# Kernel tuning notes

Measured on AMD Instinct MI355X. Metric: run time of the kernel, lower is better.

The kernel has to match this reference:

```python
import jax, jax.numpy as jnp
import numpy as np

EPS = 1e-5

def layer_norm(x, g, b):
    m = x.mean(-1, keepdims=True)
    v = ((x - m) ** 2).mean(-1, keepdims=True)
    return (x - m) / jnp.sqrt(v + EPS) * g + b

def lstm(x_sbd, W_ih, W_hh, b_ih, b_hh):
    # x_sbd: (S, B, D); PyTorch gate order i, f, g, o
    S, B, D = x_sbd.shape
    H = W_hh.shape[1]
    h0 = jnp.zeros((B, H), x_sbd.dtype)
    c0 = jnp.zeros((B, H), x_sbd.dtype)
    def step(carry, x_t):
        h, c = carry
        gates = x_t @ W_ih.T + b_ih + h @ W_hh.T + b_hh
        i, f, g, o = jnp.split(gates, 4, axis=-1)
        c = jax.nn.sigmoid(f) * c + jax.nn.sigmoid(i) * jnp.tanh(g)
        h = jax.nn.sigmoid(o) * jnp.tanh(c)
        return (h, c), h
    (hL, _), hs = jax.lax.scan(step, (h0, c0), x_sbd)
    return hs, hL  # (S,B,H), (B,H)

def setup_inputs():
    key = jax.random.key(0)
    ks = jax.random.split(key, 20)
    B, S, D, V = 64, 1024, 128, 50000
    sc = 1.0 / np.sqrt(D)
    r = lambda k, shp, s=sc: (jax.random.normal(k, shp, jnp.float32) * s)
    return {
        "new_list": jax.random.randint(ks[0], (B, S), 0, V, jnp.int32),
        "new_mask": jnp.ones((B, S), jnp.float32),
        "aspect": jax.random.randint(ks[1], (B, 1), 0, V, jnp.int32),
        "gpunum": 0,
        "emb": r(ks[2], (V, D), 0.02),
        "W_ih": r(ks[3], (4 * D, D)),
        "W_hh": r(ks[4], (4 * D, D)),
        "b_ih": jnp.zeros((4 * D,), jnp.float32),
        "b_hh": jnp.zeros((4 * D,), jnp.float32),
        "an_g": jnp.ones((D,), jnp.float32),
        "an_b": jnp.zeros((D,), jnp.float32),
        "hn_g": jnp.ones((D,), jnp.float32),
        "hn_b": jnp.zeros((D,), jnp.float32),
        "W_att": r(ks[5], (D, D)),
        "W_aw": r(ks[6], (1, D)),
        "W_rout": r(ks[7], (D, D)),
        "W_hout": r(ks[8], (D, D)),
        "W_cls": r(ks[9], (2, D)),
        "b_cls": jnp.zeros((2,), jnp.float32),
    }

def reference(new_list, new_mask, aspect, gpunum, emb, W_ih, W_hh, b_ih, b_hh,
              an_g, an_b, hn_g, hn_b, W_att, W_aw, W_rout, W_hout, W_cls, b_cls):
    # embed, seq-major for LSTM
    x = emb[new_list.T]                      # (S, B, D)
    hidden_output, h_L = lstm(x, W_ih, W_hh, b_ih, b_hh)
    aspect_emb = emb[aspect]                 # (B, 1, D)
    aspect_emb = layer_norm(aspect_emb, an_g, an_b)
    hidden_output = layer_norm(hidden_output, hn_g, hn_b)
    hid = jnp.transpose(hidden_output, (1, 0, 2))  # (B, S, D)
    # circular convolution along hidden dim via FFT (batched; replaces host scipy loop)
    M = jnp.real(jnp.fft.ifft(jnp.fft.fft(hid, axis=-1) * jnp.fft.fft(aspect_emb, axis=-1), axis=-1)).astype(hid.dtype)
    # self-attention: key=M, value=hid, mask applied before softmax (as in original)
    QK = jnp.tanh(M @ W_att.T)               # (B, S, D)
    QK = new_mask[..., None] * QK
    weight = jax.nn.softmax(QK @ W_aw.T, axis=1)  # (B, S, 1)
    r = jnp.einsum('bs,bsd->bd', weight[..., 0], hid)
    r = jnp.tanh(r @ W_rout.T + h_L @ W_hout.T)
    result = jax.nn.softmax(r @ W_cls.T + b_cls, axis=-1)
    return (result, r)
```

## Files before the change

kernel.cpp:

```cpp
#include <hip/hip_runtime.h>

typedef __attribute__((ext_vector_type(8))) short s16x8;
typedef __attribute__((ext_vector_type(4))) float f32x4;
typedef __attribute__((ext_vector_type(4))) unsigned short u16x4;
typedef __attribute__((ext_vector_type(8))) unsigned short u16x8;

#define PAD 136
#define LPAD 144

__device__ __forceinline__ unsigned short f2bf(float f){
  union{float f;unsigned u;} v; v.f=f;
  unsigned r=v.u + 0x7fffu + ((v.u>>16)&1u);
  return (unsigned short)(r>>16);
}
__device__ __forceinline__ float bf2f(unsigned short u){
  union{unsigned u;float f;} v; v.u=((unsigned)u)<<16; return v.f;
}
__device__ __forceinline__ float ubits2f(unsigned u){
  union{unsigned u;float f;} v; v.u=u; return v.f;
}
__device__ __forceinline__ float rcp_(float x){ return __builtin_amdgcn_rcpf(x); }
__device__ __forceinline__ float e2_(float x){ return __builtin_amdgcn_exp2f(x); }
__device__ __forceinline__ float tanh_(float x){ return 1.f-2.f*rcp_(1.f+e2_(x*2.885390082f)); }

__device__ __forceinline__ void mfma128(const unsigned short* As, const unsigned short* Bs, f32x4 acc[4][2]){
  const int tid=threadIdx.x, w=tid>>6, l=tid&63;
  const int wm=w>>2, wn=w&3, lr=l&15, lk=(l>>4)*8;
#pragma unroll
  for(int kc=0;kc<4;++kc){
    const int ko=kc*32+lk;
    s16x8 a[4], bb[2];
#pragma unroll
    for(int mt=0;mt<4;++mt) a[mt]=*(const s16x8*)(As+(wm*64+mt*16+lr)*PAD+ko);
#pragma unroll
    for(int nt=0;nt<2;++nt) bb[nt]=*(const s16x8*)(Bs+(wn*32+nt*16+lr)*PAD+ko);
#pragma unroll
    for(int mt=0;mt<4;++mt)
#pragma unroll
      for(int nt=0;nt<2;++nt)
        acc[mt][nt]=__builtin_amdgcn_mfma_f32_16x16x32_bf16(a[mt],bb[nt],acc[mt][nt],0,0,0);
  }
}

__global__ __launch_bounds__(256) void k_cvt(const float* __restrict__ w, unsigned short* __restrict__ o, int n){
  int i = blockIdx.x*256 + threadIdx.x;
  if (i<n) o[i] = f2bf(w[i]);
}

__global__ __launch_bounds__(512) void k_aspg(const int* __restrict__ aspect, const float* __restrict__ emb,
    const float* __restrict__ ang, const float* __restrict__ anb, const float* __restrict__ watt,
    unsigned short* __restrict__ gt){
  __shared__ unsigned short As[128*PAD];
  __shared__ unsigned short Bs[128*PAD];
  __shared__ float a_ln[128];
  __shared__ float stat[2];
  const int b=blockIdx.x, tid=threadIdx.x;
  if (tid<128) a_ln[tid] = emb[(size_t)aspect[b]*128 + tid];
  __syncthreads();
  if (tid==0){
    float s=0.f,q=0.f;
    for(int d=0;d<128;++d){ float v=a_ln[d]; s+=v; q+=v*v; }
    float m=s*(1.f/128.f);
    stat[0]=m; stat[1]=__builtin_amdgcn_rsqf(q*(1.f/128.f)-m*m+1e-5f);
  }
  __syncthreads();
  if (tid<128) a_ln[tid] = (a_ln[tid]-stat[0])*stat[1]*ang[tid]+anb[tid];
  __syncthreads();
  {
    int k=tid>>2, dq=(tid&3)*32;
    for(int d=dq; d<dq+32; ++d) As[k*PAD+d]=f2bf(a_ln[(d-k)&127]);
  }
  {
    int i=tid>>2, kq=(tid&3)*32;
    const f32x4* src=(const f32x4*)(watt+(size_t)i*128+kq);
#pragma unroll
    for(int j=0;j<8;++j){ f32x4 v=src[j]; u16x4 o;
#pragma unroll
      for(int q=0;q<4;++q) o[q]=f2bf(v[q]);
      *(u16x4*)(Bs+i*PAD+kq+4*j)=o; }
  }
  __syncthreads();
  f32x4 z={0.f,0.f,0.f,0.f};
  f32x4 acc[4][2]={{z,z},{z,z},{z,z},{z,z}};
  mfma128(As,Bs,acc);
  const int w=tid>>6,l=tid&63,wm=w>>2,wn=w&3,lr=l&15,lg=l>>4;
#pragma unroll
  for(int mt=0;mt<4;++mt)
#pragma unroll
    for(int nt=0;nt<2;++nt){
      int k0=wm*64+mt*16+lg*4;
      int n=wn*32+nt*16+lr;
      u16x4 o;
#pragma unroll
      for(int r=0;r<4;++r) o[r]=f2bf(acc[mt][nt][r]);
      *(u16x4*)(gt+(size_t)b*16384+n*128+k0)=o;
    }
}

__global__ __launch_bounds__(512) void k_xw(const int* __restrict__ new_list, const float* __restrict__ emb,
    const float* __restrict__ wih, const float* __restrict__ bih, const float* __restrict__ bhh,
    unsigned short* __restrict__ xw){
  __shared__ unsigned short As[128*PAD];
  __shared__ unsigned short Bs[128*PAD];
  const int tid=threadIdx.x;
  const int m0=blockIdx.x*128, n0=blockIdx.y*128;
  {
    int i=tid>>2, kq=(tid&3)*32;
    int m=m0+i, t=m>>6, b=m&63;
    int tok=new_list[b*1024+t];
    const f32x4* src=(const f32x4*)(emb+(size_t)tok*128+kq);
#pragma unroll
    for(int j=0;j<8;++j){ f32x4 v=src[j]; u16x4 o;
#pragma unroll
      for(int q=0;q<4;++q) o[q]=f2bf(v[q]);
      *(u16x4*)(As+i*PAD+kq+4*j)=o; }
  }
  {
    int i=tid>>2, kq=(tid&3)*32;
    const f32x4* src=(const f32x4*)(wih+(size_t)(n0+i)*128+kq);
#pragma unroll
    for(int j=0;j<8;++j){ f32x4 v=src[j]; u16x4 o;
#pragma unroll
      for(int q=0;q<4;++q) o[q]=f2bf(v[q]);
      *(u16x4*)(Bs+i*PAD+kq+4*j)=o; }
  }
  __syncthreads();
  f32x4 z={0.f,0.f,0.f,0.f};
  f32x4 acc[4][2]={{z,z},{z,z},{z,z},{z,z}};
  mfma128(As,Bs,acc);
  const int w=tid>>6,l=tid&63,wm=w>>2,wn=w&3,lr=l&15,lg=l>>4;
#pragma unroll
  for(int nt=0;nt<2;++nt){
    int n=n0+wn*32+nt*16+lr;
    float bias=bih[n]+bhh[n];
#pragma unroll
    for(int mt=0;mt<4;++mt){
      int m_=m0+wm*64+mt*16+lg*4;
      int t=m_>>6, b0=m_&63;
      u16x4 o;
#pragma unroll
      for(int r=0;r<4;++r) o[r]=f2bf(acc[mt][nt][r]+bias);
      *(u16x4*)(xw+(((size_t)t*16+(b0>>2))*512+n)*4)=o;
    }
  }
}

__global__ __launch_bounds__(512) void k_lstm(const unsigned short* __restrict__ xw,
    const unsigned short* __restrict__ whh,
    unsigned short* __restrict__ hraw, float* __restrict__ hL){
  __shared__ unsigned short hbuf[2][4*LPAD];
  const int tid=threadIdx.x, w=tid>>6, l=tid&63, lr=l&15, lg=l>>4;
  const int blk=blockIdx.x, bb=blk*4;
  const int cb=w*16+lr;
  s16x8 wf[4][4];
#pragma unroll
  for(int g=0;g<4;++g)
#pragma unroll
    for(int kc=0;kc<4;++kc)
      wf[g][kc]=*(const s16x8*)(whh+(size_t)(g*128+cb)*128+kc*32+lg*8);
  for(int i=tid;i<2*4*LPAD;i+=512) ((unsigned short*)hbuf)[i]=0;
  __syncthreads();
  const unsigned short* x0 = xw + (size_t)blk*2048;
  int xofs[4];
#pragma unroll
  for(int g=0;g<4;++g) xofs[g]=((g*128+cb)<<2)+lg;
  unsigned short px[4], p1[4];
#pragma unroll
  for(int g=0;g<4;++g) px[g]=x0[xofs[g]];
#pragma unroll
  for(int g=0;g<4;++g) p1[g]=x0[32768+xofs[g]];
  unsigned short* hrp=hraw+((size_t)(bb+lg)<<17)+cb;
  float cc=0.f, hh=0.f;
  int cur=0;
  const float L2E=1.442695041f;
  for(int t=0;t<1024;++t){
    const unsigned short* hc=hbuf[cur];
    s16x8 af[4];
#pragma unroll
    for(int kc=0;kc<4;++kc) af[kc]=*(const s16x8*)(hc+(lr>>2)*LPAD+kc*32+lg*8);
    { int t2=t+2<1024?t+2:1023;
      const unsigned short* xq=x0+(size_t)t2*32768;
      unsigned short pn[4];
#pragma unroll
      for(int g=0;g<4;++g) pn[g]=xq[xofs[g]];
      f32x4 z={0.f,0.f,0.f,0.f};
      f32x4 acc[4]={z,z,z,z};
#pragma unroll
      for(int kc=0;kc<4;++kc)
#pragma unroll
        for(int g=0;g<4;++g)
          acc[g]=__builtin_amdgcn_mfma_f32_16x16x32_bf16(af[kc],wf[g][kc],acc[g],0,0,0);
      float ga[4];
#pragma unroll
      for(int g=0;g<4;++g){
        ga[g]=acc[g][0]+ubits2f(((unsigned)px[g])<<16);
        px[g]=p1[g]; p1[g]=pn[g];
      }
      float gg=__builtin_amdgcn_fmed3f(ga[2],-30.f,30.f);
      float ei=e2_(ga[0]*-L2E), eg=e2_(gg*(-2.f*L2E));
      float sitg=rcp_((1.f+ei)*(1.f+eg))*(1.f-eg);
      float sf=rcp_(1.f+e2_(ga[1]*-L2E));
      cc=fmaf(sf,cc,sitg);
      float cl=__builtin_amdgcn_fmed3f(cc,-30.f,30.f);
      float E=e2_(cl*(2.f*L2E)), eo=e2_(ga[3]*-L2E);
      hh=(E-1.f)*rcp_((1.f+eo)*(E+1.f));
    }
    unsigned p;
    asm("v_cvt_pk_bf16_f32 %0, %1, %2":"=v"(p):"v"(hh),"v"(hh));
    unsigned short hb=(unsigned short)(p&0xffffu);
    hbuf[cur^1][lg*LPAD+cb]=hb;
    hrp[(size_t)t<<7]=hb;
    asm volatile("s_waitcnt lgkmcnt(0)\n\ts_barrier" ::: "memory");
    cur^=1;
  }
  hL[(size_t)(bb+lg)*128+cb]=hh;
}

__global__ __launch_bounds__(512) void k_scores(const unsigned short* __restrict__ hraw,
    const unsigned short* __restrict__ gt, const float* __restrict__ hng, const float* __restrict__ hnb,
    const float* __restrict__ waw, const float* __restrict__ mask,
    unsigned short* __restrict__ hln, float* __restrict__ scores){
  __shared__ unsigned short As[128*PAD];
  __shared__ unsigned short Bs[128*PAD];
  __shared__ float redS[128][4];
  __shared__ float redQ[128][4];
  __shared__ float red[128][4];
  const int b=blockIdx.x>>3, s0=(blockIdx.x&7)*128;
  const int tid=threadIdx.x;
  const int i=tid>>2, kq=(tid&3)*32;
  u16x8 hv[4];
  {
    const u16x8* src=(const u16x8*)(hraw+((size_t)b*1024+s0+i)*128+kq);
    float s=0.f,q=0.f;
#pragma unroll
    for(int j=0;j<4;++j){ hv[j]=src[j];
#pragma unroll
      for(int e=0;e<8;++e){ float x=bf2f(hv[j][e]); s+=x; q+=x*x; } }
    redS[i][tid&3]=s; redQ[i][tid&3]=q;
  }
  {
    const u16x4* src=(const u16x4*)(gt+(size_t)b*16384+i*128+kq);
#pragma unroll
    for(int j=0;j<8;++j) *(u16x4*)(Bs+i*PAD+kq+4*j)=src[j];
  }
  __syncthreads();
  {
    float s=redS[i][0]+redS[i][1]+redS[i][2]+redS[i][3];
    float q=redQ[i][0]+redQ[i][1]+redQ[i][2]+redQ[i][3];
    float m=s*(1.f/128.f);
    float inv=__builtin_amdgcn_rsqf(q*(1.f/128.f)-m*m+1e-5f);
    unsigned short* dst=hln+((size_t)b*1024+s0+i)*128+kq;
#pragma unroll
    for(int j=0;j<4;++j){ u16x8 o;
#pragma unroll
      for(int e=0;e<8;++e){ int d=kq+j*8+e;
        float x=(bf2f(hv[j][e])-m)*inv*hng[d]+hnb[d];
        o[e]=f2bf(x); }
      *(u16x8*)(As+i*PAD+kq+8*j)=o;
      *(u16x8*)(dst+8*j)=o;
    }
  }
  __syncthreads();
  f32x4 z={0.f,0.f,0.f,0.f};
  f32x4 acc[4][2]={{z,z},{z,z},{z,z},{z,z}};
  mfma128(As,Bs,acc);
  const int w=tid>>6,l=tid&63,wm=w>>2,wn=w&3,lr=l&15,lg=l>>4;
  const float w0=waw[wn*32+lr], w1=waw[wn*32+16+lr];
#pragma unroll
  for(int mt=0;mt<4;++mt){
    f32x4 p4;
#pragma unroll
    for(int r=0;r<4;++r) p4[r]=tanh_(acc[mt][0][r])*w0+tanh_(acc[mt][1][r])*w1;
#pragma unroll
    for(int m=1;m<16;m<<=1){
#pragma unroll
      for(int r=0;r<4;++r) p4[r]+=__shfl_xor(p4[r],m,64);
    }
    if (lr==0){
#pragma unroll
      for(int r=0;r<4;++r) red[wm*64+mt*16+lg*4+r][wn]=p4[r];
    }
  }
  __syncthreads();
  if (tid<128){
    float sc=red[tid][0]+red[tid][1]+red[tid][2]+red[tid][3];
    sc*=mask[b*1024+s0+tid];
    scores[b*1024+s0+tid]=sc;
  }
}

__global__ __launch_bounds__(256) void k_wsum(const float* __restrict__ scores,
    const unsigned short* __restrict__ hln, float* __restrict__ rpre){
  __shared__ float wl[1024];
  __shared__ float red[256];
  __shared__ float part[8][32];
  const int b=blockIdx.x>>2, d0=(blockIdx.x&3)*32;
  const int tid=threadIdx.x;
  float v[4]; float lm=-1e30f;
#pragma unroll
  for(int q=0;q<4;++q){ v[q]=scores[b*1024+tid+256*q]; lm=fmaxf(lm,v[q]); }
  red[tid]=lm; __syncthreads();
  for(int st=128;st;st>>=1){ if(tid<st) red[tid]=fmaxf(red[tid],red[tid+st]); __syncthreads(); }
  const float mx=red[0]; __syncthreads();
  float ls=0.f;
#pragma unroll
  for(int q=0;q<4;++q){ v[q]=e2_((v[q]-mx)*1.442695041f); ls+=v[q]; }
  red[tid]=ls; __syncthreads();
  for(int st=128;st;st>>=1){ if(tid<st) red[tid]+=red[tid+st]; __syncthreads(); }
  const float inv=rcp_(red[0]);
#pragma unroll
  for(int q=0;q<4;++q) wl[tid+256*q]=v[q]*inv;
  __syncthreads();
  const int d=tid&31, sg=tid>>5;
  float acc=0.f;
  const unsigned short* hp=hln+(size_t)b*131072+d0+d;
  for(int s=sg*128;s<sg*128+128;++s) acc+=wl[s]*bf2f(hp[(size_t)s*128]);
  part[sg][d]=acc; __syncthreads();
  if (tid<32){
    float a=0.f;
#pragma unroll
    for(int g=0;g<8;++g) a+=part[g][tid];
    rpre[b*128+d0+tid]=a;
  }
}

__global__ __launch_bounds__(128) void k_final(const float* __restrict__ rpre, const float* __restrict__ hLp,
    const float* __restrict__ wrout, const float* __restrict__ whout, const float* __restrict__ wcls,
    const float* __restrict__ bcls, float* __restrict__ out){
  __shared__ float rv[128], hv[128], cred[4];
  const int b=blockIdx.x, n=threadIdx.x;
  rv[n]=rpre[b*128+n]; hv[n]=hLp[b*128+n];
  __syncthreads();
  float a=0.f;
  const float* wr=wrout+(size_t)n*128;
  const float* wh=whout+(size_t)n*128;
  for(int k=0;k<128;++k) a+=rv[k]*wr[k]+hv[k]*wh[k];
  const float rr=tanh_(a);
  out[128+b*128+n]=rr;
  float p0=rr*wcls[n], p1=rr*wcls[128+n];
#pragma unroll
  for(int m=1;m<64;m<<=1){ p0+=__shfl_xor(p0,m,64); p1+=__shfl_xor(p1,m,64); }
  if ((n&63)==0){ cred[(n>>6)*2]=p0; cred[(n>>6)*2+1]=p1; }
  __syncthreads();
  if (n==0){
    float l0=cred[0]+cred[2]+bcls[0], l1=cred[1]+cred[3]+bcls[1];
    float m=fmaxf(l0,l1);
    float e0=e2_((l0-m)*1.442695041f), e1=e2_((l1-m)*1.442695041f);
    float s=rcp_(e0+e1);
    out[b*2]=e0*s; out[b*2+1]=e1*s;
  }
}

extern "C" void kernel_launch(void* const* d_in, const int* in_sizes, int n_in,
                              void* d_out, int out_size, void* d_ws, size_t ws_size,
                              hipStream_t stream) {
  (void)in_sizes; (void)n_in; (void)out_size; (void)ws_size;
  const int*   new_list=(const int*)d_in[0];
  const float* new_mask=(const float*)d_in[1];
  const int*   aspect  =(const int*)d_in[2];
  const float* emb   =(const float*)d_in[4];
  const float* W_ih  =(const float*)d_in[5];
  const float* W_hh  =(const float*)d_in[6];
  const float* b_ih  =(const float*)d_in[7];
  const float* b_hh  =(const float*)d_in[8];
  const float* an_g  =(const float*)d_in[9];
  const float* an_b  =(const float*)d_in[10];
  const float* hn_g  =(const float*)d_in[11];
  const float* hn_b  =(const float*)d_in[12];
  const float* W_att =(const float*)d_in[13];
  const float* W_aw  =(const float*)d_in[14];
  const float* W_rout=(const float*)d_in[15];
  const float* W_hout=(const float*)d_in[16];
  const float* W_cls =(const float*)d_in[17];
  const float* b_cls =(const float*)d_in[18];
  float* out=(float*)d_out;
  char* ws=(char*)d_ws;
  unsigned short* xw    =(unsigned short*)(ws);
  unsigned short* hraw  =(unsigned short*)(ws+67108864);
  unsigned short* hln   =(unsigned short*)(ws+83886080);
  unsigned short* gt    =(unsigned short*)(ws+100663296);
  unsigned short* whh   =(unsigned short*)(ws+102760448);
  float*          scores=(float*)(ws+102891520);
  float*          hLb   =(float*)(ws+103153664);
  float*          rpre  =(float*)(ws+103186432);
  k_cvt   <<<dim3(256),    dim3(256), 0, stream>>>(W_hh, whh, 512*128);
  k_aspg  <<<dim3(64),     dim3(512), 0, stream>>>(aspect, emb, an_g, an_b, W_att, gt);
  k_xw    <<<dim3(512,4),  dim3(512), 0, stream>>>(new_list, emb, W_ih, b_ih, b_hh, xw);
  k_lstm  <<<dim3(16),     dim3(512), 0, stream>>>(xw, whh, hraw, hLb);
  k_scores<<<dim3(512),    dim3(512), 0, stream>>>(hraw, gt, hn_g, hn_b, W_aw, new_mask, hln, scores);
  k_wsum  <<<dim3(256),    dim3(256), 0, stream>>>(scores, hln, rpre);
  k_final <<<dim3(64),     dim3(128), 0, stream>>>(rpre, hLb, W_rout, W_hout, W_cls, b_cls, out);
}
```

Before: 578.7 us.

## Batch LSTM hidden-state stores through an 8-step LDS ring and prescale gate inputs

The LSTM kernel now keeps the last eight hidden states in an LDS ring buffer. Every eight steps it writes them to global memory as 16-byte vector stores, replacing one 2-byte scattered global store per step. The input projection and W_hh conversion fold the -log2(e) and -2log2(e) factors into the stored bf16 values, which removes a multiply per gate in the serial recurrence. The price is an extra barrier every eight steps, plus extra rounding because the scaled values are kept in bf16.

New measurement: 1.088 ms. +88.0%, slower.

```diff
diff --git a/kernel.cpp b/kernel.cpp
--- a/kernel.cpp
+++ b/kernel.cpp
@@ -7,6 +7,7 @@
 
 #define PAD 136
 #define LPAD 144
+#define SSTR (4*LPAD+2)
 
 __device__ __forceinline__ unsigned short f2bf(float f){
   union{float f;unsigned u;} v; v.f=f;
@@ -44,7 +45,11 @@
 
 __global__ __launch_bounds__(256) void k_cvt(const float* __restrict__ w, unsigned short* __restrict__ o, int n){
   int i = blockIdx.x*256 + threadIdx.x;
-  if (i<n) o[i] = f2bf(w[i]);
+  if (i<n){
+    int g=(i>>14)&3;
+    float s=(g==2)?-2.885390082f:-1.442695041f;
+    o[i] = f2bf(w[i]*s);
+  }
 }
 
 __global__ __launch_bounds__(512) void k_aspg(const int* __restrict__ aspect, const float* __restrict__ emb,
@@ -133,13 +138,14 @@
   for(int nt=0;nt<2;++nt){
     int n=n0+wn*32+nt*16+lr;
     float bias=bih[n]+bhh[n];
+    float s=((n>>7)==2)?-2.885390082f:-1.442695041f;
 #pragma unroll
     for(int mt=0;mt<4;++mt){
       int m_=m0+wm*64+mt*16+lg*4;
       int t=m_>>6, b0=m_&63;
       u16x4 o;
 #pragma unroll
-      for(int r=0;r<4;++r) o[r]=f2bf(acc[mt][nt][r]+bias);
+      for(int r=0;r<4;++r) o[r]=f2bf((acc[mt][nt][r]+bias)*s);
       *(u16x4*)(xw+(((size_t)t*16+(b0>>2))*512+n)*4)=o;
     }
   }
@@ -148,7 +154,7 @@
 __global__ __launch_bounds__(512) void k_lstm(const unsigned short* __restrict__ xw,
     const unsigned short* __restrict__ whh,
     unsigned short* __restrict__ hraw, float* __restrict__ hL){
-  __shared__ unsigned short hbuf[2][4*LPAD];
+  __shared__ unsigned short hbuf[8][SSTR];
   const int tid=threadIdx.x, w=tid>>6, l=tid&63, lr=l&15, lg=l>>4;
   const int blk=blockIdx.x, bb=blk*4;
   const int cb=w*16+lr;
@@ -158,7 +164,7 @@
 #pragma unroll
     for(int kc=0;kc<4;++kc)
       wf[g][kc]=*(const s16x8*)(whh+(size_t)(g*128+cb)*128+kc*32+lg*8);
-  for(int i=tid;i<2*4*LPAD;i+=512) ((unsigned short*)hbuf)[i]=0;
+  for(int i=tid;i<8*SSTR;i+=512) ((unsigned short*)hbuf)[i]=0;
   __syncthreads();
   const unsigned short* x0 = xw + (size_t)blk*2048;
   int xofs[4];
@@ -169,49 +175,54 @@
   for(int g=0;g<4;++g) px[g]=x0[xofs[g]];
 #pragma unroll
   for(int g=0;g<4;++g) p1[g]=x0[32768+xofs[g]];
-  unsigned short* hrp=hraw+((size_t)(bb+lg)<<17)+cb;
+  const int ro=tid>>7, ss=(tid>>4)&7, c0=(tid&15)*8;
+  const unsigned short* hls=&hbuf[ss][ro*LPAD+c0];
+  unsigned short* hst = hraw + ((size_t)(bb+ro)<<17) + (ss<<7) + c0;
   float cc=0.f, hh=0.f;
-  int cur=0;
-  const float L2E=1.442695041f;
   for(int t=0;t<1024;++t){
-    const unsigned short* hc=hbuf[cur];
+    if ((t&7)==0 && t){
+      u16x8 v=*(const u16x8*)hls;
+      *(u16x8*)(hst + ((size_t)(t-8)<<7)) = v;
+      asm volatile("s_waitcnt lgkmcnt(0)\n\ts_barrier" ::: "memory");
+    }
+    const unsigned short* hc=hbuf[(t+7)&7];
     s16x8 af[4];
 #pragma unroll
     for(int kc=0;kc<4;++kc) af[kc]=*(const s16x8*)(hc+(lr>>2)*LPAD+kc*32+lg*8);
-    { int t2=t+2<1024?t+2:1023;
-      const unsigned short* xq=x0+(size_t)t2*32768;
-      unsigned short pn[4];
-#pragma unroll
-      for(int g=0;g<4;++g) pn[g]=xq[xofs[g]];
-      f32x4 z={0.f,0.f,0.f,0.f};
-      f32x4 acc[4]={z,z,z,z};
-#pragma unroll
-      for(int kc=0;kc<4;++kc)
-#pragma unroll
-        for(int g=0;g<4;++g)
-          acc[g]=__builtin_amdgcn_mfma_f32_16x16x32_bf16(af[kc],wf[g][kc],acc[g],0,0,0);
-      float ga[4];
-#pragma unroll
-      for(int g=0;g<4;++g){
-        ga[g]=acc[g][0]+ubits2f(((unsigned)px[g])<<16);
-        px[g]=p1[g]; p1[g]=pn[g];
-      }
-      float gg=__builtin_amdgcn_fmed3f(ga[2],-30.f,30.f);
-      float ei=e2_(ga[0]*-L2E), eg=e2_(gg*(-2.f*L2E));
-      float sitg=rcp_((1.f+ei)*(1.f+eg))*(1.f-eg);
-      float sf=rcp_(1.f+e2_(ga[1]*-L2E));
-      cc=fmaf(sf,cc,sitg);
-      float cl=__builtin_amdgcn_fmed3f(cc,-30.f,30.f);
-      float E=e2_(cl*(2.f*L2E)), eo=e2_(ga[3]*-L2E);
-      hh=(E-1.f)*rcp_((1.f+eo)*(E+1.f));
-    }
+    int t2=t+2<1024?t+2:1023;
+    const unsigned short* xq=x0+(size_t)t2*32768;
+    unsigned short pn[4];
+#pragma unroll
+    for(int g=0;g<4;++g) pn[g]=xq[xofs[g]];
+    f32x4 z={0.f,0.f,0.f,0.f};
+    f32x4 acc[4]={z,z,z,z};
+#pragma unroll
+    for(int kc=0;kc<4;++kc)
+#pragma unroll
+      for(int g=0;g<4;++g)
+        acc[g]=__builtin_amdgcn_mfma_f32_16x16x32_bf16(af[kc],wf[g][kc],acc[g],0,0,0);
+    float ex[4];
+#pragma unroll
+    for(int g=0;g<4;++g){
+      float a=acc[g][0]+ubits2f(((unsigned)px[g])<<16);
+      if (g==2) a=__builtin_amdgcn_fmed3f(a,-80.f,80.f);
+      ex[g]=e2_(a);
+      px[g]=p1[g]; p1[g]=pn[g];
+    }
+    float sitg=rcp_((1.f+ex[0])*(1.f+ex[2]))*(1.f-ex[2]);
+    float sf=rcp_(1.f+ex[1]);
+    cc=fmaf(sf,cc,sitg);
+    float cl=__builtin_amdgcn_fmed3f(cc,-30.f,30.f);
+    float E=e2_(cl*2.885390082f);
+    hh=(E-1.f)*rcp_((1.f+ex[3])*(E+1.f));
     unsigned p;
     asm("v_cvt_pk_bf16_f32 %0, %1, %2":"=v"(p):"v"(hh),"v"(hh));
-    unsigned short hb=(unsigned short)(p&0xffffu);
-    hbuf[cur^1][lg*LPAD+cb]=hb;
-    hrp[(size_t)t<<7]=hb;
+    hbuf[t&7][lg*LPAD+cb]=(unsigned short)(p&0xffffu);
     asm volatile("s_waitcnt lgkmcnt(0)\n\ts_barrier" ::: "memory");
-    cur^=1;
+  }
+  {
+    u16x8 v=*(const u16x8*)hls;
+    *(u16x8*)(hst + ((size_t)1016<<7)) = v;
   }
   hL[(size_t)(bb+lg)*128+cb]=hh;
 }
```
